# Performance work log

Hardware: AMD Instinct MI355X
Metric: run time of the kernel (lower is better)

Reference implementation:

```python
import jax, jax.numpy as jnp
import numpy as np

N = 50000      # num nodes
E = 800000     # num edges
IN = 128       # in_channels
OUT = 128      # out_channels
H = 8          # num_heads
HD = OUT // H  # out_channels_conv (per-head dim)
EDIM = 16      # edge_dim
HID = 512      # hidden_dim of dst MLP


def layer_norm(x, w, b, eps=1e-5):
    m = jnp.mean(x, axis=-1, keepdims=True)
    v = jnp.var(x, axis=-1, keepdims=True)
    return (x - m) * jax.lax.rsqrt(v + eps) * w + b


def setup_inputs() -> dict:
    key = jax.random.key(0)
    ks = jax.random.split(key, 16)
    lin = lambda k, i, o: jax.random.normal(k, (i, o), jnp.float32) / np.sqrt(i)
    return {
        "x": jax.random.normal(ks[0], (N, IN), jnp.float32),
        "edge_attr": jax.random.normal(ks[1], (E, EDIM), jnp.float32),
        "edge_index": jax.random.randint(ks[2], (2, E), 0, N),
        "Wq": lin(ks[3], IN, OUT), "bq": jnp.zeros((OUT,), jnp.float32),
        "Wk": lin(ks[4], IN, OUT), "bk": jnp.zeros((OUT,), jnp.float32),
        "Wv": lin(ks[5], IN, OUT), "bv": jnp.zeros((OUT,), jnp.float32),
        "Ws": lin(ks[6], IN, OUT), "bs": jnp.zeros((OUT,), jnp.float32),
        "We": lin(ks[7], EDIM, OUT), "be": jnp.zeros((OUT,), jnp.float32),
        "Wp": lin(ks[8], OUT, OUT), "bp": jnp.zeros((OUT,), jnp.float32),
        "ln_a_w": jnp.ones((IN,), jnp.float32), "ln_a_b": jnp.zeros((IN,), jnp.float32),
        "ln_m_w": jnp.ones((OUT,), jnp.float32), "ln_m_b": jnp.zeros((OUT,), jnp.float32),
        "W1": lin(ks[9], OUT, HID), "b1": jnp.zeros((HID,), jnp.float32),
        "W2": lin(ks[10], HID, OUT), "b2": jnp.zeros((OUT,), jnp.float32),
    }


def reference(x, edge_attr, edge_index, Wq, bq, Wk, bk, Wv, bv, Ws, bs, We, be,
              Wp, bp, ln_a_w, ln_a_b, ln_m_w, ln_m_b, W1, b1, W2, b2):
    src, dst = edge_index[0], edge_index[1]

    x_skip = x
    xn = layer_norm(x, ln_a_w, ln_a_b)           # pre-attention LN
    x_r = xn @ Ws + bs                           # lin_self

    q = (xn @ Wq + bq).reshape(N, H, HD)
    k = (xn @ Wk + bk).reshape(N, H, HD)
    v = (xn @ Wv + bv).reshape(N, H, HD)
    e = (edge_attr @ We + be).reshape(E, H, HD)

    # edge-indexed attention: score(edge) = <q[dst], k[src]+e> / sqrt(HD)
    kj = k[src] + e                                              # [E,H,HD]
    scores = jnp.einsum('ehd,ehd->eh', q[dst], kj) / np.sqrt(HD)  # [E,H]

    # segment softmax over incoming edges of each dst node
    smax = jax.ops.segment_max(scores, dst, num_segments=N)     # [N,H]
    smax = jnp.where(jnp.isfinite(smax), smax, 0.0)             # guard empty segments
    ex = jnp.exp(scores - smax[dst])                            # [E,H]
    denom = jax.ops.segment_sum(ex, dst, num_segments=N)        # [N,H]
    alpha = ex / jnp.maximum(denom[dst], 1e-16)                 # [E,H]

    msg = (v[src] + e) * alpha[..., None]                       # [E,H,HD]
    out = jax.ops.segment_sum(msg, dst, num_segments=N).reshape(N, OUT)

    out = (out + x_r) @ Wp + bp                                 # projection
    out = out + x_skip                                          # residual

    # dst-node MLP with pre-LN and residual
    h = layer_norm(out, ln_m_w, ln_m_b)
    nodes_new = jax.nn.gelu(h @ W1 + b1) @ W2 + b2 + out
    return nodes_new, edge_attr
```

## Files before the change

kernel.cpp:

```cpp
#include <hip/hip_runtime.h>
#include <math.h>

#define N_NODES 50000
#define N_EDGES 800000

typedef __attribute__((ext_vector_type(8))) short bf16x8;
typedef __attribute__((ext_vector_type(4))) float f32x4;

__device__ __forceinline__ short f2bf(float f){
  unsigned u = __float_as_uint(f);
  unsigned r = (u + 0x7FFFu + ((u >> 16) & 1u)) >> 16;
  return (short)r;
}
__device__ __forceinline__ unsigned pkbf(float lo, float hi){
  return (unsigned)(unsigned short)f2bf(lo) | ((unsigned)(unsigned short)f2bf(hi) << 16);
}

__device__ __forceinline__ float gelu_f(float x){
  float z = 0.7978845608028654f*(x + 0.044715f*x*x*x);
  float e = __expf(2.0f*z);
  return 0.5f*x*(2.0f - 2.0f/(e + 1.0f));
}

#define BF_LO(u) __uint_as_float((u)<<16)
#define BF_HI(u) __uint_as_float((u)&0xffff0000u)

struct Prep {
  const float* src[5]; short* dst[5];
  const float* Wq; const float* We; const float* bq;
  short* Wtqm; float* bqm;
  const float* W1; short* W1t;
  const float* W2; short* W2t;
};
__global__ __launch_bounds__(256) void k_prep(Prep a){
  int blk = blockIdx.x, tid = threadIdx.x;
  if (blk < 320){
    int b = blk >> 6;
    int i = (blk & 63)*256 + tid;
    int n = i >> 7, k = i & 127;
    a.dst[b][n*128 + k] = f2bf(a.src[b][k*128 + n]);
  } else if (blk < 384){
    int i = (blk - 320)*256 + tid;
    int k = i >> 7, j = i & 127;
    int h = j >> 4, c = j & 15;
    float s = 0.f;
    #pragma unroll
    for (int dd = 0; dd < 16; ++dd)
      s += a.Wq[k*128 + h*16 + dd] * a.We[c*128 + h*16 + dd];
    a.Wtqm[j*128 + k] = f2bf(s);
    if (k == 0){
      float t = 0.f;
      #pragma unroll
      for (int dd = 0; dd < 16; ++dd)
        t += a.bq[h*16 + dd] * a.We[c*128 + h*16 + dd];
      a.bqm[j] = t;
    }
  } else if (blk < 640){
    int i = (blk - 384)*256 + tid;
    int n = i >> 7, k = i & 127;
    a.W1t[n*128 + k] = f2bf(a.W1[k*512 + n]);
  } else {
    int i = (blk - 640)*256 + tid;
    int n = i >> 9, k = i & 511;
    a.W2t[n*512 + k] = f2bf(a.W2[k*128 + n]);
  }
}

__global__ __launch_bounds__(256) void k_deg(const int* __restrict__ dst, int* __restrict__ deg){
  int i = blockIdx.x*256 + threadIdx.x;
  if (i < N_EDGES) atomicAdd(&deg[dst[i]], 1);
}

__global__ __launch_bounds__(256) void k_bsum(const int* __restrict__ deg,
                                              int* __restrict__ bsum, int* __restrict__ hist){
  __shared__ int lhist[64];
  __shared__ int wred[4];
  int tid = threadIdx.x;
  int i = blockIdx.x*256 + tid;
  if (tid < 64) lhist[tid] = 0;
  __syncthreads();
  int v = (i < N_NODES) ? deg[i] : 0;
  if (i < N_NODES) atomicAdd(&lhist[v > 63 ? 63 : v], 1);
  int s = v;
  #pragma unroll
  for (int sh = 32; sh >= 1; sh >>= 1) s += __shfl_xor(s, sh, 64);
  if ((tid & 63) == 0) wred[tid >> 6] = s;
  __syncthreads();
  if (tid == 0) bsum[blockIdx.x] = wred[0] + wred[1] + wred[2] + wred[3];
  if (tid < 64){ int c = lhist[tid]; if (c) atomicAdd(&hist[tid], c); }
}

__global__ __launch_bounds__(256) void k_bscan(const int* __restrict__ bsum, int* __restrict__ bbase,
                                               const int* __restrict__ hist, int* __restrict__ histcur){
  __shared__ int wsum[4];
  int tid = threadIdx.x;
  int v = (tid < 196) ? bsum[tid] : 0;
  int incl = v;
  #pragma unroll
  for (int s = 1; s < 64; s <<= 1){
    int t = __shfl_up(incl, s, 64);
    if ((tid & 63) >= s) incl += t;
  }
  if ((tid & 63) == 63) wsum[tid >> 6] = incl;
  __syncthreads();
  if (tid == 0){ int c = 0; for (int j = 0; j < 4; ++j){ int t = wsum[j]; wsum[j] = c; c += t; } }
  __syncthreads();
  if (tid < 196) bbase[tid] = wsum[tid >> 6] + (incl - v);
  if (tid < 64){
    int h = hist[tid];
    int inc = h;
    #pragma unroll
    for (int s = 1; s < 64; s <<= 1){
      int t = __shfl_up(inc, s, 64);
      if (tid >= s) inc += t;
    }
    int total = __shfl(inc, 63, 64);
    histcur[tid] = total - inc;
  }
}

__global__ __launch_bounds__(256) void k_apply(const int* __restrict__ deg, const int* __restrict__ bbase,
                                               int* __restrict__ off, int* __restrict__ cursor){
  __shared__ int wsum[4];
  int tid = threadIdx.x;
  int i = blockIdx.x*256 + tid;
  int v = (i < N_NODES) ? deg[i] : 0;
  int incl = v;
  #pragma unroll
  for (int s = 1; s < 64; s <<= 1){
    int t = __shfl_up(incl, s, 64);
    if ((tid & 63) >= s) incl += t;
  }
  if ((tid & 63) == 63) wsum[tid >> 6] = incl;
  __syncthreads();
  if (tid == 0){ int c = 0; for (int j = 0; j < 4; ++j){ int t = wsum[j]; wsum[j] = c; c += t; } }
  __syncthreads();
  int excl = bbase[blockIdx.x] + wsum[tid >> 6] + (incl - v);
  if (i < N_NODES){
    off[i] = excl; cursor[i] = excl;
    if (i == N_NODES-1) off[N_NODES] = excl + v;
  }
}

__global__ __launch_bounds__(256) void k_scatter(const int* __restrict__ dst, const int* __restrict__ src,
                                                 const float* __restrict__ edge_attr,
                                                 int* __restrict__ cursor,
                                                 int* __restrict__ esrc, ushort* __restrict__ eab,
                                                 float* __restrict__ eout){
  int i = blockIdx.x*256 + threadIdx.x;
  if (i < N_EDGES){
    int d = dst[i];
    int pos = atomicAdd(&cursor[d], 1);
    esrc[pos] = src[i];
    const float* ea = edge_attr + (size_t)i*16;
    float4 a = *(const float4*)(ea+0), b = *(const float4*)(ea+4),
           c = *(const float4*)(ea+8), e = *(const float4*)(ea+12);
    uint4 o0, o1;
    o0.x = pkbf(a.x,a.y); o0.y = pkbf(a.z,a.w); o0.z = pkbf(b.x,b.y); o0.w = pkbf(b.z,b.w);
    o1.x = pkbf(c.x,c.y); o1.y = pkbf(c.z,c.w); o1.z = pkbf(e.x,e.y); o1.w = pkbf(e.z,e.w);
    *(uint4*)&eab[(size_t)pos*16]     = o0;
    *(uint4*)&eab[(size_t)pos*16 + 8] = o1;
    float* op = eout + (size_t)i*16;
    *(float4*)(op+0)  = a;
    *(float4*)(op+4)  = b;
    *(float4*)(op+8)  = c;
    *(float4*)(op+12) = e;
  }
}

__global__ __launch_bounds__(256) void k_perm(const int* __restrict__ deg, const int* __restrict__ off,
                                              int* __restrict__ histcur,
                                              int* __restrict__ perm, int2* __restrict__ rng){
  __shared__ int lhist[64];
  __shared__ int lbase[64];
  int tid = threadIdx.x;
  int i = blockIdx.x*256 + tid;
  if (tid < 64) lhist[tid] = 0;
  __syncthreads();
  int d = 0, b = 0, loc = 0;
  bool ok = i < N_NODES;
  if (ok){
    d = deg[i];
    b = d > 63 ? 63 : d;
    loc = atomicAdd(&lhist[b], 1);
  }
  __syncthreads();
  if (tid < 64){
    int c = lhist[tid];
    lbase[tid] = c ? atomicAdd(&histcur[tid], c) : 0;
  }
  __syncthreads();
  if (ok){
    int pos = lbase[b] + loc;
    perm[pos] = i;
    int o = off[i];
    rng[pos] = make_int2(o, o + d);
  }
}

__global__ __launch_bounds__(256) void k_nodeproj(
  const float* __restrict__ x, const float* __restrict__ lnw, const float* __restrict__ lnb,
  const short* __restrict__ Wtq, const short* __restrict__ Wtqm,
  const short* __restrict__ Wtk, const short* __restrict__ Wtv, const short* __restrict__ Wts,
  const float* __restrict__ bq, const float* __restrict__ bqm,
  const float* __restrict__ bk, const float* __restrict__ bv, const float* __restrict__ bs,
  ushort* __restrict__ qb, ushort* __restrict__ qweb,
  ushort* __restrict__ kb, ushort* __restrict__ vb, float* __restrict__ xr)
{
  __shared__ short A[64][136];
  int tid = threadIdx.x;
  int rbase = blockIdx.x * 64;

  {
    int r = tid >> 2, j = tid & 3;
    int row = rbase + r;
    bool ok = row < N_NODES;
    const float* xp = x + (size_t)row*128 + j*32;
    float vals[32];
    #pragma unroll
    for (int i = 0; i < 8; ++i){
      float4 t = ok ? *(const float4*)(xp + i*4) : make_float4(0,0,0,0);
      vals[i*4+0]=t.x; vals[i*4+1]=t.y; vals[i*4+2]=t.z; vals[i*4+3]=t.w;
    }
    float s = 0.f, s2 = 0.f;
    #pragma unroll
    for (int i = 0; i < 32; ++i){ s += vals[i]; s2 += vals[i]*vals[i]; }
    s  += __shfl_xor(s, 1, 64);  s  += __shfl_xor(s, 2, 64);
    s2 += __shfl_xor(s2, 1, 64); s2 += __shfl_xor(s2, 2, 64);
    float mean = s * 0.0078125f;
    float var  = s2 * 0.0078125f - mean*mean;
    float rstd = rsqrtf(var + 1e-5f);
    #pragma unroll
    for (int i = 0; i < 32; ++i){
      int col = j*32 + i;
      float xn = (vals[i]-mean)*rstd*lnw[col] + lnb[col];
      A[r][col] = f2bf(xn);
    }
  }
  __syncthreads();

  int lane = tid & 63, wave = tid >> 6;
  int row16 = lane & 15, kg = lane >> 4;
  int cb = wave * 32;

  auto gemm = [&](const short* __restrict__ B, const float* __restrict__ bias,
                  float* __restrict__ Of, ushort* __restrict__ Ob){
    f32x4 acc[4][2] = {};
    #pragma unroll
    for (int kk = 0; kk < 128; kk += 32){
      int k0 = kk + kg*8;
      bf16x8 a0 = *(const bf16x8*)&A[ 0 + row16][k0];
      bf16x8 a1 = *(const bf16x8*)&A[16 + row16][k0];
      bf16x8 a2 = *(const bf16x8*)&A[32 + row16][k0];
      bf16x8 a3 = *(const bf16x8*)&A[48 + row16][k0];
      bf16x8 b0 = *(const bf16x8*)&B[(size_t)(cb +      row16)*128 + k0];
      bf16x8 b1 = *(const bf16x8*)&B[(size_t)(cb + 16 + row16)*128 + k0];
      acc[0][0] = __builtin_amdgcn_mfma_f32_16x16x32_bf16(a0, b0, acc[0][0], 0,0,0);
      acc[1][0] = __builtin_amdgcn_mfma_f32_16x16x32_bf16(a1, b0, acc[1][0], 0,0,0);
      acc[2][0] = __builtin_amdgcn_mfma_f32_16x16x32_bf16(a2, b0, acc[2][0], 0,0,0);
      acc[3][0] = __builtin_amdgcn_mfma_f32_16x16x32_bf16(a3, b0, acc[3][0], 0,0,0);
      acc[0][1] = __builtin_amdgcn_mfma_f32_16x16x32_bf16(a0, b1, acc[0][1], 0,0,0);
      acc[1][1] = __builtin_amdgcn_mfma_f32_16x16x32_bf16(a1, b1, acc[1][1], 0,0,0);
      acc[2][1] = __builtin_amdgcn_mfma_f32_16x16x32_bf16(a2, b1, acc[2][1], 0,0,0);
      acc[3][1] = __builtin_amdgcn_mfma_f32_16x16x32_bf16(a3, b1, acc[3][1], 0,0,0);
    }
    float bv0 = bias[cb + row16], bv1 = bias[cb + 16 + row16];
    #pragma unroll
    for (int rt = 0; rt < 4; ++rt){
      #pragma unroll
      for (int i = 0; i < 4; ++i){
        int row = rbase + rt*16 + kg*4 + i;
        if (row < N_NODES){
          float v0 = acc[rt][0][i] + bv0;
          float v1 = acc[rt][1][i] + bv1;
          if (Of){
            Of[(size_t)row*128 + cb      + row16] = v0;
            Of[(size_t)row*128 + cb + 16 + row16] = v1;
          } else {
            Ob[(size_t)row*128 + cb      + row16] = (ushort)f2bf(v0);
            Ob[(size_t)row*128 + cb + 16 + row16] = (ushort)f2bf(v1);
          }
        }
      }
    }
  };
  gemm(Wtq,  bq,  nullptr, qb);
  gemm(Wtqm, bqm, nullptr, qweb);
  gemm(Wtk,  bk,  nullptr, kb);
  gemm(Wtv,  bv,  nullptr, vb);
  gemm(Wts,  bs,  xr,  nullptr);
}

__global__ __launch_bounds__(256) void k_agg(
  const ushort* __restrict__ qb, const ushort* __restrict__ qweb,
  const ushort* __restrict__ kbf, const ushort* __restrict__ vbf,
  const ushort* __restrict__ eab, const float* __restrict__ We, const float* __restrict__ be,
  const int* __restrict__ esrc, const int* __restrict__ perm, const int2* __restrict__ rng,
  float* __restrict__ xr)
{
  int tid = threadIdx.x;
  int gid = blockIdx.x*8 + (tid >> 5);
  int node = perm[gid];
  int2 r = rng[gid];
  int beg = r.x, end = r.y;
  int l = tid & 31;
  int d0 = l*4;
  int h  = l >> 2;
  int c0 = (l & 3)*4;

  uint2 qw = *(const uint2*)&qb[(size_t)node*128 + d0];
  float4 qv = make_float4(BF_LO(qw.x), BF_HI(qw.x), BF_LO(qw.y), BF_HI(qw.y));
  uint2 qew = *(const uint2*)&qweb[(size_t)node*128 + h*16 + c0];
  float4 qe = make_float4(BF_LO(qew.x), BF_HI(qew.x), BF_LO(qew.y), BF_HI(qew.y));
  float m = -INFINITY, den = 0.f;
  float4 va = make_float4(0,0,0,0);
  float4 S  = make_float4(0,0,0,0);

  int p = beg;

  int s8[8];
  {
    bool have = (beg + 8 <= end);
    #pragma unroll
    for (int j = 0; j < 8; ++j) s8[j] = have ? esrc[beg + j] : 0;
  }
  for (; p + 8 <= end; p += 8){
    int n8[8];
    bool more = (p + 16 <= end);
    #pragma unroll
    for (int j = 0; j < 8; ++j) n8[j] = more ? esrc[p + 8 + j] : 0;
    uint2 kw[8], vw[8], ew[8];
    #pragma unroll
    for (int j = 0; j < 8; ++j){
      kw[j] = *(const uint2*)&kbf[(size_t)s8[j]*128 + d0];
      vw[j] = *(const uint2*)&vbf[(size_t)s8[j]*128 + d0];
      ew[j] = *(const uint2*)&eab[(size_t)(p+j)*16 + c0];
    }
    float sc[8];
    #pragma unroll
    for (int j = 0; j < 8; ++j){
      float pp = qv.x*BF_LO(kw[j].x) + qv.y*BF_HI(kw[j].x)
               + qv.z*BF_LO(kw[j].y) + qv.w*BF_HI(kw[j].y)
               + qe.x*BF_LO(ew[j].x) + qe.y*BF_HI(ew[j].x)
               + qe.z*BF_LO(ew[j].y) + qe.w*BF_HI(ew[j].y);
      pp += __shfl_xor(pp,1,64); pp += __shfl_xor(pp,2,64);
      sc[j] = pp*0.25f;
    }
    float mn = m;
    #pragma unroll
    for (int j = 0; j < 8; ++j) mn = fmaxf(mn, sc[j]);
    float corr = __expf(m - mn);
    float w[8]; float ds = 0.f;
    #pragma unroll
    for (int j = 0; j < 8; ++j){ w[j] = __expf(sc[j]-mn); ds += w[j]; }
    den = den*corr + ds;
    float ax=0.f, ay=0.f, az=0.f, aw2=0.f, sx=0.f, sy=0.f, sz=0.f, sw=0.f;
    #pragma unroll
    for (int j = 0; j < 8; ++j){
      ax += w[j]*BF_LO(vw[j].x); ay += w[j]*BF_HI(vw[j].x);
      az += w[j]*BF_LO(vw[j].y); aw2+= w[j]*BF_HI(vw[j].y);
      sx += w[j]*BF_LO(ew[j].x); sy += w[j]*BF_HI(ew[j].x);
      sz += w[j]*BF_LO(ew[j].y); sw += w[j]*BF_HI(ew[j].y);
    }
    va.x = va.x*corr + ax; va.y = va.y*corr + ay;
    va.z = va.z*corr + az; va.w = va.w*corr + aw2;
    S.x  = S.x *corr + sx; S.y  = S.y *corr + sy;
    S.z  = S.z *corr + sz; S.w  = S.w *corr + sw;
    m = mn;
    #pragma unroll
    for (int j = 0; j < 8; ++j) s8[j] = n8[j];
  }

#define AGG_STEP(J)                                                            \
  {                                                                            \
    int sidx[J];                                                               \
    _Pragma("unroll")                                                          \
    for (int j = 0; j < J; ++j) sidx[j] = esrc[p+j];                           \
    uint2 kw[J], vw[J], ew[J];                                                 \
    _Pragma("unroll")                                                          \
    for (int j = 0; j < J; ++j){                                               \
      kw[j] = *(const uint2*)&kbf[(size_t)sidx[j]*128 + d0];                   \
      vw[j] = *(const uint2*)&vbf[(size_t)sidx[j]*128 + d0];                   \
      ew[j] = *(const uint2*)&eab[(size_t)(p+j)*16 + c0];                      \
    }                                                                          \
    float sc[J];                                                               \
    _Pragma("unroll")                                                          \
    for (int j = 0; j < J; ++j){                                               \
      float pp = qv.x*BF_LO(kw[j].x) + qv.y*BF_HI(kw[j].x)                     \
               + qv.z*BF_LO(kw[j].y) + qv.w*BF_HI(kw[j].y)                     \
               + qe.x*BF_LO(ew[j].x) + qe.y*BF_HI(ew[j].x)                     \
               + qe.z*BF_LO(ew[j].y) + qe.w*BF_HI(ew[j].y);                    \
      pp += __shfl_xor(pp,1,64); pp += __shfl_xor(pp,2,64);                    \
      sc[j] = pp*0.25f;                                                        \
    }                                                                          \
    float mn = m;                                                              \
    _Pragma("unroll")                                                          \
    for (int j = 0; j < J; ++j) mn = fmaxf(mn, sc[j]);                         \
    float corr = __expf(m - mn);                                               \
    float w[J]; float ds = 0.f;                                                \
    _Pragma("unroll")                                                          \
    for (int j = 0; j < J; ++j){ w[j] = __expf(sc[j]-mn); ds += w[j]; }        \
    den = den*corr + ds;                                                       \
    float ax=0.f, ay=0.f, az=0.f, aw2=0.f, sx=0.f, sy=0.f, sz=0.f, sw=0.f;     \
    _Pragma("unroll")                                                          \
    for (int j = 0; j < J; ++j){                                               \
      ax += w[j]*BF_LO(vw[j].x); ay += w[j]*BF_HI(vw[j].x);                    \
      az += w[j]*BF_LO(vw[j].y); aw2+= w[j]*BF_HI(vw[j].y);                    \
      sx += w[j]*BF_LO(ew[j].x); sy += w[j]*BF_HI(ew[j].x);                    \
      sz += w[j]*BF_LO(ew[j].y); sw += w[j]*BF_HI(ew[j].y);                    \
    }                                                                          \
    va.x = va.x*corr + ax; va.y = va.y*corr + ay;                              \
    va.z = va.z*corr + az; va.w = va.w*corr + aw2;                             \
    S.x  = S.x *corr + sx; S.y  = S.y *corr + sy;                              \
    S.z  = S.z *corr + sz; S.w  = S.w *corr + sw;                              \
    m = mn;                                                                    \
  }

  for (; p + 4 <= end; p += 4) AGG_STEP(4)
  for (; p < end; ++p){
    int s = esrc[p];
    uint2 kw = *(const uint2*)&kbf[(size_t)s*128 + d0];
    uint2 vw = *(const uint2*)&vbf[(size_t)s*128 + d0];
    uint2 ew = *(const uint2*)&eab[(size_t)p*16 + c0];
    float pp = qv.x*BF_LO(kw.x) + qv.y*BF_HI(kw.x)
             + qv.z*BF_LO(kw.y) + qv.w*BF_HI(kw.y)
             + qe.x*BF_LO(ew.x) + qe.y*BF_HI(ew.x)
             + qe.z*BF_LO(ew.y) + qe.w*BF_HI(ew.y);
    pp += __shfl_xor(pp,1,64); pp += __shfl_xor(pp,2,64);
    float sc = pp*0.25f;
    float mn = fmaxf(m, sc);
    float corr = __expf(m - mn);
    float pe = __expf(sc - mn);
    den = den*corr + pe;
    va.x = va.x*corr + pe*BF_LO(vw.x);
    va.y = va.y*corr + pe*BF_HI(vw.x);
    va.z = va.z*corr + pe*BF_LO(vw.y);
    va.w = va.w*corr + pe*BF_HI(vw.y);
    S.x = S.x*corr + pe*BF_LO(ew.x);
    S.y = S.y*corr + pe*BF_HI(ew.x);
    S.z = S.z*corr + pe*BF_LO(ew.y);
    S.w = S.w*corr + pe*BF_HI(ew.y);
    m = mn;
  }

  if (end > beg){
    float inv = 1.0f/den;
    float4 acc = va;
    int gb = (tid & 63) & 60;
    #pragma unroll
    for (int g = 0; g < 4; ++g){
      float s0 = __shfl(S.x, gb+g, 64);
      float s1 = __shfl(S.y, gb+g, 64);
      float s2 = __shfl(S.z, gb+g, 64);
      float s3 = __shfl(S.w, gb+g, 64);
      float4 w0 = *(const float4*)&We[(g*4+0)*128 + d0];
      float4 w1 = *(const float4*)&We[(g*4+1)*128 + d0];
      float4 w2 = *(const float4*)&We[(g*4+2)*128 + d0];
      float4 w3 = *(const float4*)&We[(g*4+3)*128 + d0];
      acc.x += s0*w0.x + s1*w1.x + s2*w2.x + s3*w3.x;
      acc.y += s0*w0.y + s1*w1.y + s2*w2.y + s3*w3.y;
      acc.z += s0*w0.z + s1*w1.z + s2*w2.z + s3*w3.z;
      acc.w += s0*w0.w + s1*w1.w + s2*w2.w + s3*w3.w;
    }
    float4 bev = *(const float4*)&be[d0];
    float4 xv = *(const float4*)&xr[(size_t)node*128 + d0];
    xv.x += acc.x*inv + bev.x;
    xv.y += acc.y*inv + bev.y;
    xv.z += acc.z*inv + bev.z;
    xv.w += acc.w*inv + bev.w;
    *(float4*)&xr[(size_t)node*128 + d0] = xv;
  }
}

__global__ __launch_bounds__(256) void k_post(
  const float* __restrict__ aggout, const float* __restrict__ x,
  const short* __restrict__ Wtp, const float* __restrict__ bp,
  const float* __restrict__ lnw, const float* __restrict__ lnb,
  float* __restrict__ res, short* __restrict__ A2)
{
  __shared__ short A[64][136];
  __shared__ float rf[64][132];
  int tid = threadIdx.x;
  int rbase = blockIdx.x * 64;

  {
    int r = tid >> 2, j = tid & 3;
    int row = rbase + r;
    const float* p = aggout + (size_t)row*128 + j*32;
    #pragma unroll
    for (int i = 0; i < 8; ++i){
      float4 t = *(const float4*)(p + i*4);
      int c = j*32 + i*4;
      A[r][c+0] = f2bf(t.x); A[r][c+1] = f2bf(t.y);
      A[r][c+2] = f2bf(t.z); A[r][c+3] = f2bf(t.w);
    }
  }
  __syncthreads();

  int lane = tid & 63, wave = tid >> 6;
  int row16 = lane & 15, kg = lane >> 4;
  int cb = wave * 32;

  f32x4 acc[4][2] = {};
  #pragma unroll
  for (int kk = 0; kk < 128; kk += 32){
    int k0 = kk + kg*8;
    bf16x8 a0 = *(const bf16x8*)&A[ 0 + row16][k0];
    bf16x8 a1 = *(const bf16x8*)&A[16 + row16][k0];
    bf16x8 a2 = *(const bf16x8*)&A[32 + row16][k0];
    bf16x8 a3 = *(const bf16x8*)&A[48 + row16][k0];
    bf16x8 b0 = *(const bf16x8*)&Wtp[(size_t)(cb +      row16)*128 + k0];
    bf16x8 b1 = *(const bf16x8*)&Wtp[(size_t)(cb + 16 + row16)*128 + k0];
    acc[0][0] = __builtin_amdgcn_mfma_f32_16x16x32_bf16(a0, b0, acc[0][0], 0,0,0);
    acc[1][0] = __builtin_amdgcn_mfma_f32_16x16x32_bf16(a1, b0, acc[1][0], 0,0,0);
    acc[2][0] = __builtin_amdgcn_mfma_f32_16x16x32_bf16(a2, b0, acc[2][0], 0,0,0);
    acc[3][0] = __builtin_amdgcn_mfma_f32_16x16x32_bf16(a3, b0, acc[3][0], 0,0,0);
    acc[0][1] = __builtin_amdgcn_mfma_f32_16x16x32_bf16(a0, b1, acc[0][1], 0,0,0);
    acc[1][1] = __builtin_amdgcn_mfma_f32_16x16x32_bf16(a1, b1, acc[1][1], 0,0,0);
    acc[2][1] = __builtin_amdgcn_mfma_f32_16x16x32_bf16(a2, b1, acc[2][1], 0,0,0);
    acc[3][1] = __builtin_amdgcn_mfma_f32_16x16x32_bf16(a3, b1, acc[3][1], 0,0,0);
  }
  float bv0 = bp[cb + row16], bv1 = bp[cb + 16 + row16];
  #pragma unroll
  for (int rt = 0; rt < 4; ++rt){
    #pragma unroll
    for (int i = 0; i < 4; ++i){
      int rl = rt*16 + kg*4 + i;
      int row = rbase + rl;
      float v0 = acc[rt][0][i] + bv0;
      float v1 = acc[rt][1][i] + bv1;
      if (row < N_NODES){
        v0 += x[(size_t)row*128 + cb      + row16];
        v1 += x[(size_t)row*128 + cb + 16 + row16];
        res[(size_t)row*128 + cb      + row16] = v0;
        res[(size_t)row*128 + cb + 16 + row16] = v1;
      }
      rf[rl][cb      + row16] = v0;
      rf[rl][cb + 16 + row16] = v1;
    }
  }
  __syncthreads();

  {
    int r = tid >> 2, j = tid & 3;
    int row = rbase + r;
    float vals[32];
    #pragma unroll
    for (int i = 0; i < 8; ++i){
      float4 t = *(const float4*)&rf[r][j*32 + i*4];
      vals[i*4+0]=t.x; vals[i*4+1]=t.y; vals[i*4+2]=t.z; vals[i*4+3]=t.w;
    }
    float s = 0.f, s2 = 0.f;
    #pragma unroll
    for (int i = 0; i < 32; ++i){ s += vals[i]; s2 += vals[i]*vals[i]; }
    s  += __shfl_xor(s, 1, 64);  s  += __shfl_xor(s, 2, 64);
    s2 += __shfl_xor(s2, 1, 64); s2 += __shfl_xor(s2, 2, 64);
    float mean = s * 0.0078125f;
    float var  = s2 * 0.0078125f - mean*mean;
    float rstd = rsqrtf(var + 1e-5f);
    #pragma unroll
    for (int i = 0; i < 32; ++i){
      int col = j*32 + i;
      float xn = (vals[i]-mean)*rstd*lnw[col] + lnb[col];
      A2[(size_t)row*128 + col] = f2bf(xn);
    }
  }
}

__global__ __launch_bounds__(256) void k_mlp1(
  const short* __restrict__ A2, const short* __restrict__ W1t, const float* __restrict__ b1,
  short* __restrict__ hid)
{
  __shared__ short A[64][136];
  int tid = threadIdx.x;
  int rbase = blockIdx.x * 64;
  int ch = blockIdx.y;
  for (int idx = tid; idx < 1024; idx += 256){
    int r = idx >> 4, g = idx & 15;
    *(uint4*)&A[r][g*8] = *(const uint4*)&A2[((size_t)(rbase + r))*128 + g*8];
  }
  __syncthreads();

  int lane = tid & 63, wave = tid >> 6;
  int row16 = lane & 15, kg = lane >> 4;
  int cb = ch*256 + wave*64;

  f32x4 acc[4][4] = {};
  #pragma unroll
  for (int kk = 0; kk < 128; kk += 32){
    int k0 = kk + kg*8;
    bf16x8 a[4], b[4];
    #pragma unroll
    for (int rt = 0; rt < 4; ++rt) a[rt] = *(const bf16x8*)&A[rt*16 + row16][k0];
    #pragma unroll
    for (int ct = 0; ct < 4; ++ct) b[ct] = *(const bf16x8*)&W1t[(size_t)(cb + ct*16 + row16)*128 + k0];
    #pragma unroll
    for (int rt = 0; rt < 4; ++rt)
      #pragma unroll
      for (int ct = 0; ct < 4; ++ct)
        acc[rt][ct] = __builtin_amdgcn_mfma_f32_16x16x32_bf16(a[rt], b[ct], acc[rt][ct], 0,0,0);
  }
  float bv[4];
  #pragma unroll
  for (int ct = 0; ct < 4; ++ct) bv[ct] = b1[cb + ct*16 + row16];
  #pragma unroll
  for (int rt = 0; rt < 4; ++rt){
    #pragma unroll
    for (int ct = 0; ct < 4; ++ct){
      #pragma unroll
      for (int i = 0; i < 4; ++i){
        int row = rbase + rt*16 + kg*4 + i;
        hid[(size_t)row*512 + cb + ct*16 + row16] = f2bf(gelu_f(acc[rt][ct][i] + bv[ct]));
      }
    }
  }
}

__global__ __launch_bounds__(256) void k_mlp2(
  const short* __restrict__ hid, const short* __restrict__ W2t, const float* __restrict__ b2,
  const float* __restrict__ res, float* __restrict__ out)
{
  __shared__ short A[64][136];
  int tid = threadIdx.x;
  int rbase = blockIdx.x * 64;
  int lane = tid & 63, wave = tid >> 6;
  int row16 = lane & 15, kg = lane >> 4;
  int cb = wave * 32;

  f32x4 acc[4][2] = {};
  for (int kc = 0; kc < 4; ++kc){
    __syncthreads();
    for (int idx = tid; idx < 1024; idx += 256){
      int r = idx >> 4, g = idx & 15;
      *(uint4*)&A[r][g*8] = *(const uint4*)&hid[((size_t)(rbase + r))*512 + kc*128 + g*8];
    }
    __syncthreads();
    #pragma unroll
    for (int kk = 0; kk < 128; kk += 32){
      int k0 = kk + kg*8;
      bf16x8 a0 = *(const bf16x8*)&A[ 0 + row16][k0];
      bf16x8 a1 = *(const bf16x8*)&A[16 + row16][k0];
      bf16x8 a2 = *(const bf16x8*)&A[32 + row16][k0];
      bf16x8 a3 = *(const bf16x8*)&A[48 + row16][k0];
      bf16x8 b0 = *(const bf16x8*)&W2t[(size_t)(cb +      row16)*512 + kc*128 + k0];
      bf16x8 b1 = *(const bf16x8*)&W2t[(size_t)(cb + 16 + row16)*512 + kc*128 + k0];
      acc[0][0] = __builtin_amdgcn_mfma_f32_16x16x32_bf16(a0, b0, acc[0][0], 0,0,0);
      acc[1][0] = __builtin_amdgcn_mfma_f32_16x16x32_bf16(a1, b0, acc[1][0], 0,0,0);
      acc[2][0] = __builtin_amdgcn_mfma_f32_16x16x32_bf16(a2, b0, acc[2][0], 0,0,0);
      acc[3][0] = __builtin_amdgcn_mfma_f32_16x16x32_bf16(a3, b0, acc[3][0], 0,0,0);
      acc[0][1] = __builtin_amdgcn_mfma_f32_16x16x32_bf16(a0, b1, acc[0][1], 0,0,0);
      acc[1][1] = __builtin_amdgcn_mfma_f32_16x16x32_bf16(a1, b1, acc[1][1], 0,0,0);
      acc[2][1] = __builtin_amdgcn_mfma_f32_16x16x32_bf16(a2, b1, acc[2][1], 0,0,0);
      acc[3][1] = __builtin_amdgcn_mfma_f32_16x16x32_bf16(a3, b1, acc[3][1], 0,0,0);
    }
  }
  float bv0 = b2[cb + row16], bv1 = b2[cb + 16 + row16];
  #pragma unroll
  for (int rt = 0; rt < 4; ++rt){
    #pragma unroll
    for (int i = 0; i < 4; ++i){
      int row = rbase + rt*16 + kg*4 + i;
      if (row < N_NODES){
        out[(size_t)row*128 + cb      + row16] = acc[rt][0][i] + bv0 + res[(size_t)row*128 + cb      + row16];
        out[(size_t)row*128 + cb + 16 + row16] = acc[rt][1][i] + bv1 + res[(size_t)row*128 + cb + 16 + row16];
      }
    }
  }
}

extern "C" void kernel_launch(void* const* d_in, const int* in_sizes, int n_in,
                              void* d_out, int out_size, void* d_ws, size_t ws_size,
                              hipStream_t stream)
{
  const float* x        = (const float*)d_in[0];
  const float* edge_attr= (const float*)d_in[1];
  const int*   edge_index=(const int*)d_in[2];
  const float* Wq = (const float*)d_in[3];  const float* bq = (const float*)d_in[4];
  const float* Wk = (const float*)d_in[5];  const float* bk = (const float*)d_in[6];
  const float* Wv = (const float*)d_in[7];  const float* bv = (const float*)d_in[8];
  const float* Wss= (const float*)d_in[9];  const float* bss= (const float*)d_in[10];
  const float* We = (const float*)d_in[11]; const float* be = (const float*)d_in[12];
  const float* Wp = (const float*)d_in[13]; const float* bp = (const float*)d_in[14];
  const float* lnaw=(const float*)d_in[15]; const float* lnab=(const float*)d_in[16];
  const float* lnmw=(const float*)d_in[17]; const float* lnmb=(const float*)d_in[18];
  const float* W1 = (const float*)d_in[19]; const float* b1 = (const float*)d_in[20];
  const float* W2 = (const float*)d_in[21]; const float* b2 = (const float*)d_in[22];

  float* ws = (float*)d_ws;
  const size_t NP128 = 6406144;
  const size_t NPH   = 3203072;
  ushort* qb   = (ushort*)ws;
  ushort* qweb = (ushort*)(ws + NPH);
  ushort* kbf  = (ushort*)(ws + 2*NPH);
  ushort* vbf  = (ushort*)(ws + 3*NPH);
  float*  xr   = ws + 4*NPH;
  float*  res  = ws + 4*NPH + NP128;
  ushort* eab  = (ushort*)res;
  short* wts   = (short*)(ws + 25624576);
  short* Wtq   = wts;
  short* Wtk   = wts + 16384;
  short* Wtv   = wts + 32768;
  short* Wts_  = wts + 49152;
  short* Wtp   = wts + 65536;
  short* Wtqm  = wts + 81920;
  short* W1t   = wts + 98304;
  short* W2t   = wts + 163840;
  float* bqm   = ws + 25624576 + 114688 + 16384;
  int*   iw    = (int*)(bqm + 128);
  int* deg     = iw;
  int* hist    = iw + 50000;
  int* histcur = iw + 50064;
  int* bsum    = iw + 50128;
  int* bbase   = iw + 50324;
  int* off     = iw + 50520;
  int* cursor  = iw + 100521;
  int* perm    = iw + 150521;
  int2* rng    = (int2*)(iw + 200522);
  int* esrc    = iw + 300522;

  short* A2   = (short*)qb;
  short* hid  = (short*)qweb;

  const int* srcIdx = edge_index;
  const int* dstIdx = edge_index + N_EDGES;

  Prep pa;
  pa.src[0]=Wq; pa.src[1]=Wk; pa.src[2]=Wv; pa.src[3]=Wss; pa.src[4]=Wp;
  pa.dst[0]=Wtq; pa.dst[1]=Wtk; pa.dst[2]=Wtv; pa.dst[3]=Wts_; pa.dst[4]=Wtp;
  pa.Wq=Wq; pa.We=We; pa.bq=bq; pa.Wtqm=Wtqm; pa.bqm=bqm;
  pa.W1=W1; pa.W1t=W1t; pa.W2=W2; pa.W2t=W2t;
  k_prep<<<896, 256, 0, stream>>>(pa);

  hipMemsetAsync(deg, 0, 50064*sizeof(int), stream);
  k_deg<<<(N_EDGES+255)/256, 256, 0, stream>>>(dstIdx, deg);
  k_bsum<<<196, 256, 0, stream>>>(deg, bsum, hist);
  k_bscan<<<1, 256, 0, stream>>>(bsum, bbase, hist, histcur);
  k_apply<<<196, 256, 0, stream>>>(deg, bbase, off, cursor);
  k_scatter<<<(N_EDGES+255)/256, 256, 0, stream>>>(dstIdx, srcIdx, edge_attr, cursor, esrc, eab,
                                                   (float*)d_out + (size_t)N_NODES*128);
  k_perm<<<(N_NODES+255)/256, 256, 0, stream>>>(deg, off, histcur, perm, rng);

  k_nodeproj<<<782, 256, 0, stream>>>(x, lnaw, lnab, Wtq, Wtqm, Wtk, Wtv, Wts_,
                                      bq, bqm, bk, bv, bss, qb, qweb, kbf, vbf, xr);
  k_agg<<<N_NODES/8, 256, 0, stream>>>(qb, qweb, kbf, vbf, eab, We, be,
                                       esrc, perm, rng, xr);
  k_post<<<782, 256, 0, stream>>>(xr, x, Wtp, bp, lnmw, lnmb, res, A2);
  k_mlp1<<<dim3(782,2), 256, 0, stream>>>(A2, W1t, b1, hid);
  k_mlp2<<<782, 256, 0, stream>>>(hid, W2t, b2, res, (float*)d_out);
}
```

Before: 343.9 us.

## Fuse post-projection, LN and MLP into one kernel; store self/agg output in bf16

Merges k_post, k_mlp1 and k_mlp2 into a single k_postmlp kernel working on 32-row tiles, so the residual, normalized activations and 512-wide hidden layer stay in shared memory instead of going through global memory. The lin_self/aggregation buffer xr is now kept in bf16 rather than fp32, which halves its traffic. k_apply and k_perm are also merged, which drops one launch and the off array. The costs are extra rounding of the aggregated output to bf16 and much higher shared memory per block, which may limit occupancy.

```diff
diff --git a/kernel.cpp b/kernel.cpp
--- a/kernel.cpp
+++ b/kernel.cpp
@@ -119,11 +119,16 @@
   }
 }
 
-__global__ __launch_bounds__(256) void k_apply(const int* __restrict__ deg, const int* __restrict__ bbase,
-                                               int* __restrict__ off, int* __restrict__ cursor){
+__global__ __launch_bounds__(256) void k_applyperm(
+  const int* __restrict__ deg, const int* __restrict__ bbase, int* __restrict__ histcur,
+  int* __restrict__ cursor, int* __restrict__ perm, int2* __restrict__ rng)
+{
   __shared__ int wsum[4];
+  __shared__ int lhist[64];
+  __shared__ int lbase[64];
   int tid = threadIdx.x;
   int i = blockIdx.x*256 + tid;
+  if (tid < 64) lhist[tid] = 0;
   int v = (i < N_NODES) ? deg[i] : 0;
   int incl = v;
   #pragma unroll
@@ -136,9 +141,23 @@
   if (tid == 0){ int c = 0; for (int j = 0; j < 4; ++j){ int t = wsum[j]; wsum[j] = c; c += t; } }
   __syncthreads();
   int excl = bbase[blockIdx.x] + wsum[tid >> 6] + (incl - v);
-  if (i < N_NODES){
-    off[i] = excl; cursor[i] = excl;
-    if (i == N_NODES-1) off[N_NODES] = excl + v;
+  bool ok = i < N_NODES;
+  int b = 0, loc = 0;
+  if (ok){
+    cursor[i] = excl;
+    b = v > 63 ? 63 : v;
+    loc = atomicAdd(&lhist[b], 1);
+  }
+  __syncthreads();
+  if (tid < 64){
+    int c = lhist[tid];
+    lbase[tid] = c ? atomicAdd(&histcur[tid], c) : 0;
+  }
+  __syncthreads();
+  if (ok){
+    int pos = lbase[b] + loc;
+    perm[pos] = i;
+    rng[pos] = make_int2(excl, excl + v);
   }
 }
 
@@ -168,36 +187,6 @@
   }
 }
 
-__global__ __launch_bounds__(256) void k_perm(const int* __restrict__ deg, const int* __restrict__ off,
-                                              int* __restrict__ histcur,
-                                              int* __restrict__ perm, int2* __restrict__ rng){
-  __shared__ int lhist[64];
-  __shared__ int lbase[64];
-  int tid = threadIdx.x;
-  int i = blockIdx.x*256 + tid;
-  if (tid < 64) lhist[tid] = 0;
-  __syncthreads();
-  int d = 0, b = 0, loc = 0;
-  bool ok = i < N_NODES;
-  if (ok){
-    d = deg[i];
-    b = d > 63 ? 63 : d;
-    loc = atomicAdd(&lhist[b], 1);
-  }
-  __syncthreads();
-  if (tid < 64){
-    int c = lhist[tid];
-    lbase[tid] = c ? atomicAdd(&histcur[tid], c) : 0;
-  }
-  __syncthreads();
-  if (ok){
-    int pos = lbase[b] + loc;
-    perm[pos] = i;
-    int o = off[i];
-    rng[pos] = make_int2(o, o + d);
-  }
-}
-
 __global__ __launch_bounds__(256) void k_nodeproj(
   const float* __restrict__ x, const float* __restrict__ lnw, const float* __restrict__ lnb,
   const short* __restrict__ Wtq, const short* __restrict__ Wtqm,
@@ -205,7 +194,7 @@
   const float* __restrict__ bq, const float* __restrict__ bqm,
   const float* __restrict__ bk, const float* __restrict__ bv, const float* __restrict__ bs,
   ushort* __restrict__ qb, ushort* __restrict__ qweb,
-  ushort* __restrict__ kb, ushort* __restrict__ vb, float* __restrict__ xr)
+  ushort* __restrict__ kb, ushort* __restrict__ vb, ushort* __restrict__ xrb)
 {
   __shared__ short A[64][136];
   int tid = threadIdx.x;
@@ -244,7 +233,7 @@
   int cb = wave * 32;
 
   auto gemm = [&](const short* __restrict__ B, const float* __restrict__ bias,
-                  float* __restrict__ Of, ushort* __restrict__ Ob){
+                  ushort* __restrict__ Ob){
     f32x4 acc[4][2] = {};
     #pragma unroll
     for (int kk = 0; kk < 128; kk += 32){
@@ -271,24 +260,17 @@
       for (int i = 0; i < 4; ++i){
         int row = rbase + rt*16 + kg*4 + i;
         if (row < N_NODES){
-          float v0 = acc[rt][0][i] + bv0;
-          float v1 = acc[rt][1][i] + bv1;
-          if (Of){
-            Of[(size_t)row*128 + cb      + row16] = v0;
-            Of[(size_t)row*128 + cb + 16 + row16] = v1;
-          } else {
-            Ob[(size_t)row*128 + cb      + row16] = (ushort)f2bf(v0);
-            Ob[(size_t)row*128 + cb + 16 + row16] = (ushort)f2bf(v1);
-          }
+          Ob[(size_t)row*128 + cb      + row16] = (ushort)f2bf(acc[rt][0][i] + bv0);
+          Ob[(size_t)row*128 + cb + 16 + row16] = (ushort)f2bf(acc[rt][1][i] + bv1);
         }
       }
     }
   };
-  gemm(Wtq,  bq,  nullptr, qb);
-  gemm(Wtqm, bqm, nullptr, qweb);
-  gemm(Wtk,  bk,  nullptr, kb);
-  gemm(Wtv,  bv,  nullptr, vb);
-  gemm(Wts,  bs,  xr,  nullptr);
+  gemm(Wtq,  bq,  qb);
+  gemm(Wtqm, bqm, qweb);
+  gemm(Wtk,  bk,  kb);
+  gemm(Wtv,  bv,  vb);
+  gemm(Wts,  bs,  xrb);
 }
 
 __global__ __launch_bounds__(256) void k_agg(
@@ -296,7 +278,7 @@
   const ushort* __restrict__ kbf, const ushort* __restrict__ vbf,
   const ushort* __restrict__ eab, const float* __restrict__ We, const float* __restrict__ be,
   const int* __restrict__ esrc, const int* __restrict__ perm, const int2* __restrict__ rng,
-  float* __restrict__ xr)
+  ushort* __restrict__ xrb)
 {
   int tid = threadIdx.x;
   int gid = blockIdx.x*8 + (tid >> 5);
@@ -463,206 +445,153 @@
       acc.w += s0*w0.w + s1*w1.w + s2*w2.w + s3*w3.w;
     }
     float4 bev = *(const float4*)&be[d0];
-    float4 xv = *(const float4*)&xr[(size_t)node*128 + d0];
+    uint2 xw = *(const uint2*)&xrb[(size_t)node*128 + d0];
+    float4 xv = make_float4(BF_LO(xw.x), BF_HI(xw.x), BF_LO(xw.y), BF_HI(xw.y));
     xv.x += acc.x*inv + bev.x;
     xv.y += acc.y*inv + bev.y;
     xv.z += acc.z*inv + bev.z;
     xv.w += acc.w*inv + bev.w;
-    *(float4*)&xr[(size_t)node*128 + d0] = xv;
-  }
-}
-
-__global__ __launch_bounds__(256) void k_post(
-  const float* __restrict__ aggout, const float* __restrict__ x,
+    uint2 ow;
+    ow.x = pkbf(xv.x, xv.y);
+    ow.y = pkbf(xv.z, xv.w);
+    *(uint2*)&xrb[(size_t)node*128 + d0] = ow;
+  }
+}
+
+__global__ __launch_bounds__(256) void k_postmlp(
+  const ushort* __restrict__ aggout, const float* __restrict__ x,
   const short* __restrict__ Wtp, const float* __restrict__ bp,
   const float* __restrict__ lnw, const float* __restrict__ lnb,
-  float* __restrict__ res, short* __restrict__ A2)
+  const short* __restrict__ W1t, const float* __restrict__ b1,
+  const short* __restrict__ W2t, const float* __restrict__ b2,
+  float* __restrict__ out)
 {
-  __shared__ short A[64][136];
-  __shared__ float rf[64][132];
+  __shared__ short A[32][136];
+  __shared__ float rf[32][132];
+  __shared__ short Hd[32][520];
   int tid = threadIdx.x;
-  int rbase = blockIdx.x * 64;
-
-  {
-    int r = tid >> 2, j = tid & 3;
-    int row = rbase + r;
-    const float* p = aggout + (size_t)row*128 + j*32;
-    #pragma unroll
-    for (int i = 0; i < 8; ++i){
-      float4 t = *(const float4*)(p + i*4);
-      int c = j*32 + i*4;
-      A[r][c+0] = f2bf(t.x); A[r][c+1] = f2bf(t.y);
-      A[r][c+2] = f2bf(t.z); A[r][c+3] = f2bf(t.w);
-    }
-  }
-  __syncthreads();
-
+  int rbase = blockIdx.x * 32;
   int lane = tid & 63, wave = tid >> 6;
   int row16 = lane & 15, kg = lane >> 4;
-  int cb = wave * 32;
-
-  f32x4 acc[4][2] = {};
-  #pragma unroll
-  for (int kk = 0; kk < 128; kk += 32){
-    int k0 = kk + kg*8;
-    bf16x8 a0 = *(const bf16x8*)&A[ 0 + row16][k0];
-    bf16x8 a1 = *(const bf16x8*)&A[16 + row16][k0];
-    bf16x8 a2 = *(const bf16x8*)&A[32 + row16][k0];
-    bf16x8 a3 = *(const bf16x8*)&A[48 + row16][k0];
-    bf16x8 b0 = *(const bf16x8*)&Wtp[(size_t)(cb +      row16)*128 + k0];
-    bf16x8 b1 = *(const bf16x8*)&Wtp[(size_t)(cb + 16 + row16)*128 + k0];
-    acc[0][0] = __builtin_amdgcn_mfma_f32_16x16x32_bf16(a0, b0, acc[0][0], 0,0,0);
-    acc[1][0] = __builtin_amdgcn_mfma_f32_16x16x32_bf16(a1, b0, acc[1][0], 0,0,0);
-    acc[2][0] = __builtin_amdgcn_mfma_f32_16x16x32_bf16(a2, b0, acc[2][0], 0,0,0);
-    acc[3][0] = __builtin_amdgcn_mfma_f32_16x16x32_bf16(a3, b0, acc[3][0], 0,0,0);
-    acc[0][1] = __builtin_amdgcn_mfma_f32_16x16x32_bf16(a0, b1, acc[0][1], 0,0,0);
-    acc[1][1] = __builtin_amdgcn_mfma_f32_16x16x32_bf16(a1, b1, acc[1][1], 0,0,0);
-    acc[2][1] = __builtin_amdgcn_mfma_f32_16x16x32_bf16(a2, b1, acc[2][1], 0,0,0);
-    acc[3][1] = __builtin_amdgcn_mfma_f32_16x16x32_bf16(a3, b1, acc[3][1], 0,0,0);
-  }
-  float bv0 = bp[cb + row16], bv1 = bp[cb + 16 + row16];
-  #pragma unroll
-  for (int rt = 0; rt < 4; ++rt){
+
+  for (int idx = tid; idx < 512; idx += 256){
+    int r = idx >> 4, g = idx & 15;
+    *(uint4*)&A[r][g*8] = *(const uint4*)&aggout[((size_t)(rbase + r))*128 + g*8];
+  }
+  __syncthreads();
+
+  {
+    int cb = wave * 32;
+    f32x4 acc[2][2] = {};
+    #pragma unroll
+    for (int kk = 0; kk < 128; kk += 32){
+      int k0 = kk + kg*8;
+      bf16x8 a0 = *(const bf16x8*)&A[     row16][k0];
+      bf16x8 a1 = *(const bf16x8*)&A[16 + row16][k0];
+      bf16x8 b0 = *(const bf16x8*)&Wtp[(size_t)(cb +      row16)*128 + k0];
+      bf16x8 b1 = *(const bf16x8*)&Wtp[(size_t)(cb + 16 + row16)*128 + k0];
+      acc[0][0] = __builtin_amdgcn_mfma_f32_16x16x32_bf16(a0, b0, acc[0][0], 0,0,0);
+      acc[1][0] = __builtin_amdgcn_mfma_f32_16x16x32_bf16(a1, b0, acc[1][0], 0,0,0);
+      acc[0][1] = __builtin_amdgcn_mfma_f32_16x16x32_bf16(a0, b1, acc[0][1], 0,0,0);
+      acc[1][1] = __builtin_amdgcn_mfma_f32_16x16x32_bf16(a1, b1, acc[1][1], 0,0,0);
+    }
+    float bv0 = bp[cb + row16], bv1 = bp[cb + 16 + row16];
+    #pragma unroll
+    for (int rt = 0; rt < 2; ++rt){
+      #pragma unroll
+      for (int i = 0; i < 4; ++i){
+        int rl = rt*16 + kg*4 + i;
+        int row = rbase + rl;
+        float v0 = acc[rt][0][i] + bv0;
+        float v1 = acc[rt][1][i] + bv1;
+        if (row < N_NODES){
+          v0 += x[(size_t)row*128 + cb      + row16];
+          v1 += x[(size_t)row*128 + cb + 16 + row16];
+        }
+        rf[rl][cb      + row16] = v0;
+        rf[rl][cb + 16 + row16] = v1;
+      }
+    }
+  }
+  __syncthreads();
+
+  {
+    int r = tid >> 3, j = tid & 7;
+    float vals[16];
     #pragma unroll
     for (int i = 0; i < 4; ++i){
-      int rl = rt*16 + kg*4 + i;
-      int row = rbase + rl;
-      float v0 = acc[rt][0][i] + bv0;
-      float v1 = acc[rt][1][i] + bv1;
-      if (row < N_NODES){
-        v0 += x[(size_t)row*128 + cb      + row16];
-        v1 += x[(size_t)row*128 + cb + 16 + row16];
-        res[(size_t)row*128 + cb      + row16] = v0;
-        res[(size_t)row*128 + cb + 16 + row16] = v1;
-      }
-      rf[rl][cb      + row16] = v0;
-      rf[rl][cb + 16 + row16] = v1;
-    }
-  }
-  __syncthreads();
-
-  {
-    int r = tid >> 2, j = tid & 3;
-    int row = rbase + r;
-    float vals[32];
-    #pragma unroll
-    for (int i = 0; i < 8; ++i){
-      float4 t = *(const float4*)&rf[r][j*32 + i*4];
+      float4 t = *(const float4*)&rf[r][j*16 + i*4];
       vals[i*4+0]=t.x; vals[i*4+1]=t.y; vals[i*4+2]=t.z; vals[i*4+3]=t.w;
     }
     float s = 0.f, s2 = 0.f;
     #pragma unroll
-    for (int i = 0; i < 32; ++i){ s += vals[i]; s2 += vals[i]*vals[i]; }
-    s  += __shfl_xor(s, 1, 64);  s  += __shfl_xor(s, 2, 64);
-    s2 += __shfl_xor(s2, 1, 64); s2 += __shfl_xor(s2, 2, 64);
+    for (int i = 0; i < 16; ++i){ s += vals[i]; s2 += vals[i]*vals[i]; }
+    s  += __shfl_xor(s, 1, 64);  s  += __shfl_xor(s, 2, 64);  s  += __shfl_xor(s, 4, 64);
+    s2 += __shfl_xor(s2, 1, 64); s2 += __shfl_xor(s2, 2, 64); s2 += __shfl_xor(s2, 4, 64);
     float mean = s * 0.0078125f;
     float var  = s2 * 0.0078125f - mean*mean;
     float rstd = rsqrtf(var + 1e-5f);
     #pragma unroll
-    for (int i = 0; i < 32; ++i){
-      int col = j*32 + i;
-      float xn = (vals[i]-mean)*rstd*lnw[col] + lnb[col];
-      A2[(size_t)row*128 + col] = f2bf(xn);
-    }
-  }
-}
-
-__global__ __launch_bounds__(256) void k_mlp1(
-  const short* __restrict__ A2, const short* __restrict__ W1t, const float* __restrict__ b1,
-  short* __restrict__ hid)
-{
-  __shared__ short A[64][136];
-  int tid = threadIdx.x;
-  int rbase = blockIdx.x * 64;
-  int ch = blockIdx.y;
-  for (int idx = tid; idx < 1024; idx += 256){
-    int r = idx >> 4, g = idx & 15;
-    *(uint4*)&A[r][g*8] = *(const uint4*)&A2[((size_t)(rbase + r))*128 + g*8];
-  }
-  __syncthreads();
-
-  int lane = tid & 63, wave = tid >> 6;
-  int row16 = lane & 15, kg = lane >> 4;
-  int cb = ch*256 + wave*64;
-
-  f32x4 acc[4][4] = {};
-  #pragma unroll
-  for (int kk = 0; kk < 128; kk += 32){
-    int k0 = kk + kg*8;
-    bf16x8 a[4], b[4];
-    #pragma unroll
-    for (int rt = 0; rt < 4; ++rt) a[rt] = *(const bf16x8*)&A[rt*16 + row16][k0];
-    #pragma unroll
-    for (int ct = 0; ct < 4; ++ct) b[ct] = *(const bf16x8*)&W1t[(size_t)(cb + ct*16 + row16)*128 + k0];
-    #pragma unroll
-    for (int rt = 0; rt < 4; ++rt)
+    for (int i = 0; i < 16; ++i){
+      int col = j*16 + i;
+      A[r][col] = f2bf((vals[i]-mean)*rstd*lnw[col] + lnb[col]);
+    }
+  }
+  __syncthreads();
+
+  {
+    f32x4 acc[2][8] = {};
+    #pragma unroll
+    for (int kk = 0; kk < 128; kk += 32){
+      int k0 = kk + kg*8;
+      bf16x8 a0 = *(const bf16x8*)&A[     row16][k0];
+      bf16x8 a1 = *(const bf16x8*)&A[16 + row16][k0];
       #pragma unroll
-      for (int ct = 0; ct < 4; ++ct)
-        acc[rt][ct] = __builtin_amdgcn_mfma_f32_16x16x32_bf16(a[rt], b[ct], acc[rt][ct], 0,0,0);
-  }
-  float bv[4];
-  #pragma unroll
-  for (int ct = 0; ct < 4; ++ct) bv[ct] = b1[cb + ct*16 + row16];
-  #pragma unroll
-  for (int rt = 0; rt < 4; ++rt){
-    #pragma unroll
-    for (int ct = 0; ct < 4; ++ct){
+      for (int ct = 0; ct < 8; ++ct){
+        bf16x8 b = *(const bf16x8*)&W1t[(size_t)(wave*128 + ct*16 + row16)*128 + k0];
+        acc[0][ct] = __builtin_amdgcn_mfma_f32_16x16x32_bf16(a0, b, acc[0][ct], 0,0,0);
+        acc[1][ct] = __builtin_amdgcn_mfma_f32_16x16x32_bf16(a1, b, acc[1][ct], 0,0,0);
+      }
+    }
+    #pragma unroll
+    for (int ct = 0; ct < 8; ++ct){
+      int col = wave*128 + ct*16 + row16;
+      float bb = b1[col];
+      #pragma unroll
+      for (int rt = 0; rt < 2; ++rt)
+        #pragma unroll
+        for (int i = 0; i < 4; ++i)
+          Hd[rt*16 + kg*4 + i][col] = f2bf(gelu_f(acc[rt][ct][i] + bb));
+    }
+  }
+  __syncthreads();
+
+  {
+    int cb = wave * 32;
+    f32x4 acc[2][2] = {};
+    #pragma unroll
+    for (int kc = 0; kc < 16; ++kc){
+      int k0 = kc*32 + kg*8;
+      bf16x8 a0 = *(const bf16x8*)&Hd[     row16][k0];
+      bf16x8 a1 = *(const bf16x8*)&Hd[16 + row16][k0];
+      bf16x8 b0 = *(const bf16x8*)&W2t[(size_t)(cb +      row16)*512 + k0];
+      bf16x8 b1 = *(const bf16x8*)&W2t[(size_t)(cb + 16 + row16)*512 + k0];
+      acc[0][0] = __builtin_amdgcn_mfma_f32_16x16x32_bf16(a0, b0, acc[0][0], 0,0,0);
+      acc[1][0] = __builtin_amdgcn_mfma_f32_16x16x32_bf16(a1, b0, acc[1][0], 0,0,0);
+      acc[0][1] = __builtin_amdgcn_mfma_f32_16x16x32_bf16(a0, b1, acc[0][1], 0,0,0);
+      acc[1][1] = __builtin_amdgcn_mfma_f32_16x16x32_bf16(a1, b1, acc[1][1], 0,0,0);
+    }
+    float bv0 = b2[cb + row16], bv1 = b2[cb + 16 + row16];
+    #pragma unroll
+    for (int rt = 0; rt < 2; ++rt){
       #pragma unroll
       for (int i = 0; i < 4; ++i){
-        int row = rbase + rt*16 + kg*4 + i;
-        hid[(size_t)row*512 + cb + ct*16 + row16] = f2bf(gelu_f(acc[rt][ct][i] + bv[ct]));
-      }
-    }
-  }
-}
-
-__global__ __launch_bounds__(256) void k_mlp2(
-  const short* __restrict__ hid, const short* __restrict__ W2t, const float* __restrict__ b2,
-  const float* __restrict__ res, float* __restrict__ out)
-{
-  __shared__ short A[64][136];
-  int tid = threadIdx.x;
-  int rbase = blockIdx.x * 64;
-  int lane = tid & 63, wave = tid >> 6;
-  int row16 = lane & 15, kg = lane >> 4;
-  int cb = wave * 32;
-
-  f32x4 acc[4][2] = {};
-  for (int kc = 0; kc < 4; ++kc){
-    __syncthreads();
-    for (int idx = tid; idx < 1024; idx += 256){
-      int r = idx >> 4, g = idx & 15;
-      *(uint4*)&A[r][g*8] = *(const uint4*)&hid[((size_t)(rbase + r))*512 + kc*128 + g*8];
-    }
-    __syncthreads();
-    #pragma unroll
-    for (int kk = 0; kk < 128; kk += 32){
-      int k0 = kk + kg*8;
-      bf16x8 a0 = *(const bf16x8*)&A[ 0 + row16][k0];
-      bf16x8 a1 = *(const bf16x8*)&A[16 + row16][k0];
-      bf16x8 a2 = *(const bf16x8*)&A[32 + row16][k0];
-      bf16x8 a3 = *(const bf16x8*)&A[48 + row16][k0];
-      bf16x8 b0 = *(const bf16x8*)&W2t[(size_t)(cb +      row16)*512 + kc*128 + k0];
-      bf16x8 b1 = *(const bf16x8*)&W2t[(size_t)(cb + 16 + row16)*512 + kc*128 + k0];
-      acc[0][0] = __builtin_amdgcn_mfma_f32_16x16x32_bf16(a0, b0, acc[0][0], 0,0,0);
-      acc[1][0] = __builtin_amdgcn_mfma_f32_16x16x32_bf16(a1, b0, acc[1][0], 0,0,0);
-      acc[2][0] = __builtin_amdgcn_mfma_f32_16x16x32_bf16(a2, b0, acc[2][0], 0,0,0);
-      acc[3][0] = __builtin_amdgcn_mfma_f32_16x16x32_bf16(a3, b0, acc[3][0], 0,0,0);
-      acc[0][1] = __builtin_amdgcn_mfma_f32_16x16x32_bf16(a0, b1, acc[0][1], 0,0,0);
-      acc[1][1] = __builtin_amdgcn_mfma_f32_16x16x32_bf16(a1, b1, acc[1][1], 0,0,0);
-      acc[2][1] = __builtin_amdgcn_mfma_f32_16x16x32_bf16(a2, b1, acc[2][1], 0,0,0);
-      acc[3][1] = __builtin_amdgcn_mfma_f32_16x16x32_bf16(a3, b1, acc[3][1], 0,0,0);
-    }
-  }
-  float bv0 = b2[cb + row16], bv1 = b2[cb + 16 + row16];
-  #pragma unroll
-  for (int rt = 0; rt < 4; ++rt){
-    #pragma unroll
-    for (int i = 0; i < 4; ++i){
-      int row = rbase + rt*16 + kg*4 + i;
-      if (row < N_NODES){
-        out[(size_t)row*128 + cb      + row16] = acc[rt][0][i] + bv0 + res[(size_t)row*128 + cb      + row16];
-        out[(size_t)row*128 + cb + 16 + row16] = acc[rt][1][i] + bv1 + res[(size_t)row*128 + cb + 16 + row16];
+        int rl = rt*16 + kg*4 + i;
+        int row = rbase + rl;
+        if (row < N_NODES){
+          out[(size_t)row*128 + cb      + row16] = acc[rt][0][i] + bv0 + rf[rl][cb      + row16];
+          out[(size_t)row*128 + cb + 16 + row16] = acc[rt][1][i] + bv1 + rf[rl][cb + 16 + row16];
+        }
       }
     }
   }
@@ -687,15 +616,13 @@
   const float* W2 = (const float*)d_in[21]; const float* b2 = (const float*)d_in[22];
 
   float* ws = (float*)d_ws;
-  const size_t NP128 = 6406144;
-  const size_t NPH   = 3203072;
+  const size_t NPH = 3203072;
   ushort* qb   = (ushort*)ws;
   ushort* qweb = (ushort*)(ws + NPH);
   ushort* kbf  = (ushort*)(ws + 2*NPH);
   ushort* vbf  = (ushort*)(ws + 3*NPH);
-  float*  xr   = ws + 4*NPH;
-  float*  res  = ws + 4*NPH + NP128;
-  ushort* eab  = (ushort*)res;
+  ushort* xrb  = (ushort*)(ws + 4*NPH);
+  ushort* eab  = (ushort*)(ws + 5*NPH);
   short* wts   = (short*)(ws + 25624576);
   short* Wtq   = wts;
   short* Wtk   = wts + 16384;
@@ -712,14 +639,10 @@
   int* histcur = iw + 50064;
   int* bsum    = iw + 50128;
   int* bbase   = iw + 50324;
-  int* off     = iw + 50520;
-  int* cursor  = iw + 100521;
-  int* perm    = iw + 150521;
-  int2* rng    = (int2*)(iw + 200522);
-  int* esrc    = iw + 300522;
-
-  short* A2   = (short*)qb;
-  short* hid  = (short*)qweb;
+  int* cursor  = iw + 50520;
+  int* perm    = iw + 100520;
+  int2* rng    = (int2*)(iw + 150520);
+  int* esrc    = iw + 250520;
 
   const int* srcIdx = edge_index;
   const int* dstIdx = edge_index + N_EDGES;
@@ -735,16 +658,14 @@
   k_deg<<<(N_EDGES+255)/256, 256, 0, stream>>>(dstIdx, deg);
   k_bsum<<<196, 256, 0, stream>>>(deg, bsum, hist);
   k_bscan<<<1, 256, 0, stream>>>(bsum, bbase, hist, histcur);
-  k_apply<<<196, 256, 0, stream>>>(deg, bbase, off, cursor);
+  k_applyperm<<<196, 256, 0, stream>>>(deg, bbase, histcur, cursor, perm, rng);
   k_scatter<<<(N_EDGES+255)/256, 256, 0, stream>>>(dstIdx, srcIdx, edge_attr, cursor, esrc, eab,
                                                    (float*)d_out + (size_t)N_NODES*128);
-  k_perm<<<(N_NODES+255)/256, 256, 0, stream>>>(deg, off, histcur, perm, rng);
 
   k_nodeproj<<<782, 256, 0, stream>>>(x, lnaw, lnab, Wtq, Wtqm, Wtk, Wtv, Wts_,
-                                      bq, bqm, bk, bv, bss, qb, qweb, kbf, vbf, xr);
+                                      bq, bqm, bk, bv, bss, qb, qweb, kbf, vbf, xrb);
   k_agg<<<N_NODES/8, 256, 0, stream>>>(qb, qweb, kbf, vbf, eab, We, be,
-                                       esrc, perm, rng, xr);
-  k_post<<<782, 256, 0, stream>>>(xr, x, Wtp, bp, lnmw, lnmb, res, A2);
-  k_mlp1<<<dim3(782,2), 256, 0, stream>>>(A2, W1t, b1, hid);
-  k_mlp2<<<782, 256, 0, stream>>>(hid, W2t, b2, res, (float*)d_out);
-}
+                                       esrc, perm, rng, xrb);
+  k_postmlp<<<1564, 256, 0, stream>>>(xrb, x, Wtp, bp, lnmw, lnmb,
+                                      W1t, b1, W2t, b2, (float*)d_out);
+}
```

Measured after the change: 325.6 us. 1.06x faster.
